# Optimization experiments

Measured on AMD Instinct MI355X. Metric: run time of the kernel, lower is better.

## Reference

```python
import jax, jax.numpy as jnp
import numpy as np

NUM_ROIS = 100
FLAT = NUM_ROIS * NUM_ROIS
B = 16
EPS_LN = 1e-5
NEG_SLOPE = 0.2
MASK_NEG = -1e9


def _normal(key, shape, scale):
    return (jax.random.normal(key, shape, dtype=jnp.float32) * scale)


def setup_inputs() -> dict:
    key = jax.random.key(0)
    ks = jax.random.split(key, 32)
    inp = {}
    inp["raw_fc_flat"] = jax.random.normal(ks[0], (B, FLAT), dtype=jnp.float32)
    # graph builder Linear(FLAT, FLAT)
    inp["gb_W"] = _normal(ks[1], (FLAT, FLAT), 1.0 / np.sqrt(FLAT))
    inp["gb_b"] = jnp.zeros((FLAT,), jnp.float32)
    # feature enhancer: Linear(2,8) -> GELU -> Linear(8,16) -> LayerNorm(16)
    inp["fe_W1"] = _normal(ks[2], (2, 8), 1.0 / np.sqrt(2))
    inp["fe_b1"] = jnp.zeros((8,), jnp.float32)
    inp["fe_W2"] = _normal(ks[3], (8, 16), 1.0 / np.sqrt(8))
    inp["fe_b2"] = jnp.zeros((16,), jnp.float32)
    inp["fe_g"] = jnp.ones((16,), jnp.float32)
    inp["fe_beta"] = jnp.zeros((16,), jnp.float32)
    # GATv2 layer 1: in=16, C=128, H=8, concat
    H1, C1 = 8, 128
    inp["Wl1"] = _normal(ks[4], (16, H1 * C1), 1.0 / np.sqrt(16))
    inp["bl1"] = jnp.zeros((H1 * C1,), jnp.float32)
    inp["Wr1"] = _normal(ks[5], (16, H1 * C1), 1.0 / np.sqrt(16))
    inp["br1"] = jnp.zeros((H1 * C1,), jnp.float32)
    inp["att1"] = _normal(ks[6], (H1, C1), 1.0 / np.sqrt(C1))
    inp["bias1"] = jnp.zeros((H1 * C1,), jnp.float32)
    # GATv2 layer 2: in=1024, C=256, H=4, concat
    H2, C2 = 4, 256
    inp["Wl2"] = _normal(ks[7], (1024, H2 * C2), 1.0 / np.sqrt(1024))
    inp["bl2"] = jnp.zeros((H2 * C2,), jnp.float32)
    inp["Wr2"] = _normal(ks[8], (1024, H2 * C2), 1.0 / np.sqrt(1024))
    inp["br2"] = jnp.zeros((H2 * C2,), jnp.float32)
    inp["att2"] = _normal(ks[9], (H2, C2), 1.0 / np.sqrt(C2))
    inp["bias2"] = jnp.zeros((H2 * C2,), jnp.float32)
    # GATv2 layer 3: in=1024, C=128, H=1, concat=False
    H3, C3 = 1, 128
    inp["Wl3"] = _normal(ks[10], (1024, H3 * C3), 1.0 / np.sqrt(1024))
    inp["bl3"] = jnp.zeros((H3 * C3,), jnp.float32)
    inp["Wr3"] = _normal(ks[11], (1024, H3 * C3), 1.0 / np.sqrt(1024))
    inp["br3"] = jnp.zeros((H3 * C3,), jnp.float32)
    inp["att3"] = _normal(ks[12], (H3, C3), 1.0 / np.sqrt(C3))
    inp["bias3"] = jnp.zeros((C3,), jnp.float32)
    return inp


def _gelu(x):
    return jax.nn.gelu(x, approximate=False)


def _gatv2(x, mask, Wl, bl, Wr, br, att, bias, concat):
    # x: [B,N,Fin], mask: [B,N,N] bool, mask[b,i,j] = edge j->i exists (i = target)
    b, n, _ = x.shape
    h, c = att.shape
    xl = (x @ Wl + bl).reshape(b, n, h, c)  # source / message features
    xr = (x @ Wr + br).reshape(b, n, h, c)  # target features
    # GATv2 score: e[b,h,i,j] = att_h . LeakyReLU(xl[b,j,h] + xr[b,i,h])
    g = jax.nn.leaky_relu(xl[:, None, :, :, :] + xr[:, :, None, :, :], NEG_SLOPE)  # [B,i,j,H,C]
    e = jnp.einsum('bijhc,hc->bhij', g, att)
    e = jnp.where(mask[:, None], e, MASK_NEG)
    alpha = jax.nn.softmax(e, axis=-1)
    alpha = jnp.where(mask[:, None], alpha, 0.0)  # zero rows with no neighbors
    out = jnp.einsum('bhij,bjhc->bihc', alpha, xl)  # [B,N,H,C]
    out = out.reshape(b, n, h * c) if concat else out.mean(axis=2)
    return out + bias


def reference(raw_fc_flat, gb_W, gb_b, fe_W1, fe_b1, fe_W2, fe_b2, fe_g, fe_beta,
              Wl1, bl1, Wr1, br1, att1, bias1,
              Wl2, bl2, Wr2, br2, att2, bias2,
              Wl3, bl3, Wr3, br3, att3, bias3):
    bs = raw_fc_flat.shape[0]
    n = NUM_ROIS
    # --- build_graph ---
    adj = jax.nn.sigmoid(raw_fc_flat @ gb_W + gb_b).reshape(bs, n, n)
    adj = (adj + jnp.swapaxes(adj, 1, 2)) * 0.5
    m = adj.mean(axis=2)                 # per-row mean   [B,N]
    s = adj.std(axis=2, ddof=1)          # unbiased std   [B,N]
    b_ft = jnp.stack([m, s + 1e-6], axis=-1)  # [B,N,2]
    hft = _gelu(b_ft @ fe_W1 + fe_b1) @ fe_W2 + fe_b2  # [B,N,16]
    mu = hft.mean(axis=-1, keepdims=True)
    var = hft.var(axis=-1, keepdims=True)
    x = (hft - mu) / jnp.sqrt(var + EPS_LN) * fe_g + fe_beta  # node features [B,N,16]
    thr = jnp.quantile(adj.reshape(bs, -1), 0.75, axis=1)      # per-sample threshold [B]
    mask = adj > thr[:, None, None]  # symmetric edge mask [B,N,N]
    eye = jnp.eye(n, dtype=bool)[None]
    mask_sl = mask | eye  # layers 2,3 add self loops
    # --- GAT stack (eval mode: dropout = identity) ---
    x = _gelu(_gatv2(x, mask, Wl1, bl1, Wr1, br1, att1, bias1, concat=True))
    x = _gelu(_gatv2(x, mask_sl, Wl2, bl2, Wr2, br2, att2, bias2, concat=True))
    x = _gelu(_gatv2(x, mask_sl, Wl3, bl3, Wr3, br3, att3, bias3, concat=False))
    # global mean pool over nodes of each graph
    return x.mean(axis=1)  # [B, gnn_output_dim]
```

## Files before the change

### kernel.cpp

```cpp
#include <hip/hip_runtime.h>
#include <cmath>

#define BATCH 16
#define NROI 100
#define FLATD 10000
#define NTILE 10

typedef __attribute__((ext_vector_type(8))) short s16x8;
typedef __attribute__((ext_vector_type(4))) short s16x4;
typedef __attribute__((ext_vector_type(4))) float f32x4;

__device__ __forceinline__ float sigmoidf(float x) { return 1.0f / (1.0f + expf(-x)); }
__device__ __forceinline__ float geluf(float x) { return 0.5f * x * (1.0f + erff(x * 0.70710678118654752f)); }
__device__ __forceinline__ short f2bf(float x) {
    union { float f; unsigned u; } v; v.f = x;
    unsigned r = v.u + 0x7FFF + ((v.u >> 16) & 1);
    return (short)(r >> 16);
}

__global__ __launch_bounds__(256) void prep_misc(const float* __restrict__ A, float* __restrict__ At,
                                                 const float* __restrict__ Wl2, const float* __restrict__ Wr2,
                                                 const float* __restrict__ Wl3, const float* __restrict__ Wr3,
                                                 short* __restrict__ Wt2l, short* __restrict__ Wt2r,
                                                 short* __restrict__ Wt3l, short* __restrict__ Wt3r) {
    __shared__ float t[32][33];
    int bid = blockIdx.x;
    int tid = threadIdx.x;
    if (bid < 625) {
        int e = bid * 256 + tid;
        At[e] = A[(size_t)(e & 15) * FLATD + (e >> 4)];
        return;
    }
    int r = bid - 625;
    const float* in; short* out; int N, xb, yb;
    if (r < 1024)      { in = Wl2; out = Wt2l; N = 1024; xb = r & 31; yb = r >> 5; }
    else if (r < 2048) { r -= 1024; in = Wr2; out = Wt2r; N = 1024; xb = r & 31; yb = r >> 5; }
    else if (r < 2176) { r -= 2048; in = Wl3; out = Wt3l; N = 128;  xb = r & 3;  yb = r >> 2; }
    else               { r -= 2176; in = Wr3; out = Wt3r; N = 128;  xb = r & 3;  yb = r >> 2; }
    int n0 = xb * 32, k0 = yb * 32;
    int tx = tid & 31, ty = tid >> 5;
#pragma unroll
    for (int i = 0; i < 32; i += 8)
        t[ty + i][tx] = in[(size_t)(k0 + ty + i) * N + n0 + tx];
    __syncthreads();
#pragma unroll
    for (int i = 0; i < 32; i += 8)
        out[(size_t)(n0 + ty + i) * 1024 + k0 + tx] = f2bf(t[tx][ty + i]);
}

__global__ __launch_bounds__(256) void gemm1_part(const float* __restrict__ At, const float* __restrict__ W,
                                                  float* __restrict__ part) {
    int col = blockIdx.x * 512 + threadIdx.x * 2;
    if (col >= FLATD) return;
    int ky = blockIdx.y;
    int k0 = ky * 400, k1 = k0 + 400;
    float acc0[16], acc1[16];
#pragma unroll
    for (int m = 0; m < 16; ++m) { acc0[m] = 0.f; acc1[m] = 0.f; }
#pragma unroll 4
    for (int k = k0; k < k1; ++k) {
        float2 w = *reinterpret_cast<const float2*>(W + (size_t)k * FLATD + col);
        const float* a = At + k * 16;
#pragma unroll
        for (int m = 0; m < 16; ++m) { acc0[m] += a[m] * w.x; acc1[m] += a[m] * w.y; }
    }
    float* dst = part + (size_t)ky * 160000;
#pragma unroll
    for (int m = 0; m < 16; ++m) {
        float2 o; o.x = acc0[m]; o.y = acc1[m];
        *reinterpret_cast<float2*>(dst + (size_t)m * FLATD + col) = o;
    }
}

__global__ __launch_bounds__(256) void sym_stats(const float* __restrict__ part, const float* __restrict__ gbb,
                                                 float* __restrict__ adjsym, float* __restrict__ bft) {
    __shared__ float s_adj[50][NROI + 1];
    int b = blockIdx.x;
    int i0 = blockIdx.y * 50;
    for (int idx = threadIdx.x; idx < 50 * NROI; idx += 256) {
        int ii = idx / NROI, j = idx % NROI;
        int i = i0 + ii;
        size_t e1 = (size_t)b * FLATD + i * NROI + j;
        size_t e2 = (size_t)b * FLATD + j * NROI + i;
        float s1 = 0.f, s2 = 0.f;
#pragma unroll
        for (int p = 0; p < 25; ++p) {
            s1 += part[(size_t)p * 160000 + e1];
            s2 += part[(size_t)p * 160000 + e2];
        }
        float v = 0.5f * (sigmoidf(s1 + gbb[i * NROI + j]) + sigmoidf(s2 + gbb[j * NROI + i]));
        s_adj[ii][j] = v;
        adjsym[e1] = v;
    }
    __syncthreads();
    if (threadIdx.x < 50) {
        int i = threadIdx.x;
        float sum = 0.f, sumsq = 0.f;
        for (int j = 0; j < NROI; ++j) { float v = s_adj[i][j]; sum += v; sumsq += v * v; }
        float mean = sum * 0.01f;
        float var = (sumsq - sum * sum * 0.01f) * (1.0f / 99.0f);
        var = fmaxf(var, 0.f);
        bft[(b * NROI + i0 + i) * 2 + 0] = mean;
        bft[(b * NROI + i0 + i) * 2 + 1] = sqrtf(var) + 1e-6f;
    }
}

__global__ __launch_bounds__(512) void quant_enh(const float* __restrict__ adjsym, float* __restrict__ thr,
                                                 const float* __restrict__ bft,
                                                 const float* __restrict__ W1, const float* __restrict__ b1,
                                                 const float* __restrict__ W2, const float* __restrict__ b2,
                                                 const float* __restrict__ g, const float* __restrict__ beta,
                                                 float* __restrict__ x0) {
    if (blockIdx.x >= 16) {
        int idx = (blockIdx.x - 16) * 512 + threadIdx.x;
        if (idx >= BATCH * NROI) return;
        float f0 = bft[idx * 2 + 0], f1 = bft[idx * 2 + 1];
        float h8[8];
#pragma unroll
        for (int u = 0; u < 8; ++u) h8[u] = geluf(W1[u] * f0 + W1[8 + u] * f1 + b1[u]);
        float o[16];
        float mu = 0.f;
#pragma unroll
        for (int v = 0; v < 16; ++v) {
            float t = b2[v];
#pragma unroll
            for (int u = 0; u < 8; ++u) t += h8[u] * W2[u * 16 + v];
            o[v] = t; mu += t;
        }
        mu *= (1.0f / 16.0f);
        float var = 0.f;
#pragma unroll
        for (int v = 0; v < 16; ++v) { float d = o[v] - mu; var += d * d; }
        var *= (1.0f / 16.0f);
        float inv = rsqrtf(var + 1e-5f);
#pragma unroll
        for (int v = 0; v < 16; ++v) x0[idx * 16 + v] = (o[v] - mu) * inv * g[v] + beta[v];
        return;
    }
    __shared__ int red[8];
    __shared__ float redf[8];
    int b = blockIdx.x;
    int tid = threadIdx.x;
    unsigned v[20];
    const unsigned* src = (const unsigned*)(adjsym + (size_t)b * FLATD);
#pragma unroll
    for (int s = 0; s < 20; ++s) {
        int idx = s * 512 + tid;
        v[s] = (idx < FLATD) ? src[idx] : 0x7F800000u;
    }
    int rem = 7499;
    unsigned prefix = 0;
    for (int bit = 30; bit >= 0; --bit) {
        unsigned pshift = prefix >> (bit + 1);
        int c = 0;
#pragma unroll
        for (int s = 0; s < 20; ++s) {
            unsigned x = v[s];
            c += (((x >> (bit + 1)) == pshift) && (((x >> bit) & 1u) == 0u)) ? 1 : 0;
        }
#pragma unroll
        for (int o = 32; o > 0; o >>= 1) c += __shfl_down(c, o, 64);
        if ((tid & 63) == 0) red[tid >> 6] = c;
        __syncthreads();
        int total = red[0] + red[1] + red[2] + red[3] + red[4] + red[5] + red[6] + red[7];
        __syncthreads();
        if (rem >= total) { rem -= total; prefix |= 1u << bit; }
    }
    union { unsigned u; float f; } cv; cv.u = prefix;
    float v0 = cv.f;
    int cle = 0;
    float mg = 3.4e38f;
#pragma unroll
    for (int s = 0; s < 20; ++s) {
        union { unsigned u; float f; } w; w.u = v[s];
        float f = w.f;
        cle += (f <= v0) ? 1 : 0;
        if (f > v0) mg = fminf(mg, f);
    }
#pragma unroll
    for (int o = 32; o > 0; o >>= 1) {
        cle += __shfl_down(cle, o, 64);
        mg = fminf(mg, __shfl_down(mg, o, 64));
    }
    if ((tid & 63) == 0) { red[tid >> 6] = cle; redf[tid >> 6] = mg; }
    __syncthreads();
    if (tid == 0) {
        int tc = 0; float tm = 3.4e38f;
#pragma unroll
        for (int w = 0; w < 8; ++w) { tc += red[w]; tm = fminf(tm, redf[w]); }
        float v1 = (tc >= 7501) ? v0 : tm;
        thr[b] = v0 + 0.25f * (v1 - v0);
    }
}

__global__ __launch_bounds__(256) void proj_gemm(const float* __restrict__ X,
                                                 const float* __restrict__ WL, const float* __restrict__ WR,
                                                 const float* __restrict__ biasL, const float* __restrict__ biasR,
                                                 float* __restrict__ outL, float* __restrict__ outR,
                                                 int K, int Nout) {
    __shared__ float As[16][65];
    __shared__ float Bs[16][128];
    const float* W = blockIdx.z ? WR : WL;
    const float* bias = blockIdx.z ? biasR : biasL;
    float* out = blockIdx.z ? outR : outL;
    int tid = threadIdx.x;
    int tm = tid & 15, tn = tid >> 4;
    int m0 = blockIdx.x * 64, n0 = blockIdx.y * 128;
    float acc[4][8];
#pragma unroll
    for (int r = 0; r < 4; ++r)
#pragma unroll
        for (int c = 0; c < 8; ++c) acc[r][c] = 0.f;
    for (int k0 = 0; k0 < K; k0 += 16) {
        for (int e = tid; e < 64 * 16; e += 256) {
            int kk = e & 15, mm = e >> 4;
            As[kk][mm] = X[(size_t)(m0 + mm) * K + k0 + kk];
        }
        for (int e = tid; e < 16 * 128; e += 256) {
            int nn = e & 127, kk = e >> 7;
            Bs[kk][nn] = W[(size_t)(k0 + kk) * Nout + n0 + nn];
        }
        __syncthreads();
#pragma unroll
        for (int kk = 0; kk < 16; ++kk) {
            float a[4], bb[8];
#pragma unroll
            for (int r = 0; r < 4; ++r) a[r] = As[kk][tm * 4 + r];
#pragma unroll
            for (int c = 0; c < 8; ++c) bb[c] = Bs[kk][tn * 8 + c];
#pragma unroll
            for (int r = 0; r < 4; ++r)
#pragma unroll
                for (int c = 0; c < 8; ++c) acc[r][c] += a[r] * bb[c];
        }
        __syncthreads();
    }
#pragma unroll
    for (int r = 0; r < 4; ++r)
#pragma unroll
        for (int c = 0; c < 8; ++c)
            out[(size_t)(m0 + tm * 4 + r) * Nout + n0 + tn * 8 + c] = acc[r][c] + bias[n0 + tn * 8 + c];
}

__global__ __launch_bounds__(256) void mfma_proj(const short* __restrict__ Xb,
                                                 const short* __restrict__ WtL, const short* __restrict__ WtR,
                                                 const float* __restrict__ biasL, const float* __restrict__ biasR,
                                                 float* __restrict__ outL, float* __restrict__ outR,
                                                 int K, int N) {
    __shared__ short As[64 * 72];
    __shared__ short Bs[64 * 72];
    const short* Wt  = blockIdx.z ? WtR : WtL;
    const float* bias = blockIdx.z ? biasR : biasL;
    float* out = blockIdx.z ? outR : outL;
    int m0 = blockIdx.x * 64, n0 = blockIdx.y * 64;
    int tid = threadIdx.x;
    int row = tid >> 2, part = tid & 3;
    int lane = tid & 63, wave = tid >> 6;
    int wm = wave & 1, wn = wave >> 1;
    int quad = lane >> 4, l16 = lane & 15;
    f32x4 acc00 = {}, acc01 = {}, acc10 = {}, acc11 = {};
    const short* gA = Xb + (size_t)(m0 + row) * K + part * 16;
    const short* gB = Wt + (size_t)(n0 + row) * K + part * 16;
    short* sA = As + row * 72 + part * 16;
    short* sB = Bs + row * 72 + part * 16;
    const short* fA = As + (wm * 32 + l16) * 72 + quad * 8;
    const short* fB = Bs + (wn * 32 + l16) * 72 + quad * 8;
    for (int k0 = 0; k0 < K; k0 += 64) {
        *reinterpret_cast<s16x8*>(sA)     = *reinterpret_cast<const s16x8*>(gA + k0);
        *reinterpret_cast<s16x8*>(sA + 8) = *reinterpret_cast<const s16x8*>(gA + k0 + 8);
        *reinterpret_cast<s16x8*>(sB)     = *reinterpret_cast<const s16x8*>(gB + k0);
        *reinterpret_cast<s16x8*>(sB + 8) = *reinterpret_cast<const s16x8*>(gB + k0 + 8);
        __syncthreads();
#pragma unroll
        for (int ks = 0; ks < 2; ++ks) {
            s16x8 a0 = *reinterpret_cast<const s16x8*>(fA + ks * 32);
            s16x8 a1 = *reinterpret_cast<const s16x8*>(fA + ks * 32 + 16 * 72);
            s16x8 b0 = *reinterpret_cast<const s16x8*>(fB + ks * 32);
            s16x8 b1 = *reinterpret_cast<const s16x8*>(fB + ks * 32 + 16 * 72);
            acc00 = __builtin_amdgcn_mfma_f32_16x16x32_bf16(a0, b0, acc00, 0, 0, 0);
            acc01 = __builtin_amdgcn_mfma_f32_16x16x32_bf16(a0, b1, acc01, 0, 0, 0);
            acc10 = __builtin_amdgcn_mfma_f32_16x16x32_bf16(a1, b0, acc10, 0, 0, 0);
            acc11 = __builtin_amdgcn_mfma_f32_16x16x32_bf16(a1, b1, acc11, 0, 0, 0);
        }
        __syncthreads();
    }
#pragma unroll
    for (int tm = 0; tm < 2; ++tm)
#pragma unroll
        for (int tn = 0; tn < 2; ++tn) {
            const f32x4& a = tm == 0 ? (tn == 0 ? acc00 : acc01) : (tn == 0 ? acc10 : acc11);
            int mbase = m0 + wm * 32 + tm * 16 + quad * 4;
            int n = n0 + wn * 32 + tn * 16 + l16;
            float bv = bias[n];
#pragma unroll
            for (int r = 0; r < 4; ++r)
                out[(size_t)(mbase + r) * N + n] = a[r] + bv;
        }
}

__global__ __launch_bounds__(128) void score_softmax(const float* __restrict__ xl, const float* __restrict__ xr,
                                                     const float* __restrict__ att, const float* __restrict__ adjsym,
                                                     const float* __restrict__ thr, float* __restrict__ alpha,
                                                     int H, int C, int self_loop) {
    __shared__ float s_abs[NTILE][105];
    __shared__ float dl_lds[104];
    int bh = blockIdx.x;
    int b = bh / H, h = bh % H;
    int i0 = blockIdx.y * NTILE;
    int j = threadIdx.x;
    const float* xlrow = xl + ((size_t)(b * NROI + (j < NROI ? j : 0)) * H + h) * C;
    const float* xrbase = xr + ((size_t)(b * NROI + i0) * H + h) * C;
    const float* atth = att + h * C;
    float acc[NTILE];
    float dl = 0.f;
#pragma unroll
    for (int i = 0; i < NTILE; ++i) acc[i] = 0.f;
    for (int cc = 0; cc < C; cc += 32) {
        float xlr[32];
#pragma unroll
        for (int t = 0; t < 32; ++t) xlr[t] = xlrow[cc + t];
        const float* attp = atth + cc;
#pragma unroll
        for (int t = 0; t < 32; ++t) dl += attp[t] * xlr[t];
#pragma unroll
        for (int i = 0; i < NTILE; ++i) {
            const float* xrrow = xrbase + (size_t)i * H * C + cc;
            float s = 0.f;
#pragma unroll
            for (int t = 0; t < 32; ++t) s += attp[t] * fabsf(xlr[t] + xrrow[t]);
            acc[i] += s;
        }
    }
    if (j < NROI) {
        dl_lds[j] = dl;
#pragma unroll
        for (int i = 0; i < NTILE; ++i) s_abs[i][j] = acc[i];
    }
    __syncthreads();
    int t = threadIdx.x;
    int i = t >> 2, q = t & 3;
    if (i < NTILE) {
        int gi = i0 + i;
        int c4 = C >> 2;
        const float* xrrow = xr + ((size_t)(b * NROI + gi) * H + h) * C + q * c4;
        const float* attq = atth + q * c4;
        float dr = 0.f;
        for (int c = 0; c < c4; ++c) dr += attq[c] * xrrow[c];
        dr += __shfl_xor(dr, 1, 64);
        dr += __shfl_xor(dr, 2, 64);
        float tb = thr[b];
        const float* arow = adjsym + (size_t)b * FLATD + gi * NROI + q * 25;
        float em[25];
        float mx = -3.0e38f;
#pragma unroll
        for (int k = 0; k < 25; ++k) {
            int jj = q * 25 + k;
            float e = 0.6f * (dl_lds[jj] + dr) + 0.4f * s_abs[i][jj];
            bool edge = (arow[k] > tb) || (self_loop && (jj == gi));
            float v = edge ? e : -1.0e9f;
            em[k] = v;
            mx = fmaxf(mx, v);
        }
        mx = fmaxf(mx, __shfl_xor(mx, 1, 64));
        mx = fmaxf(mx, __shfl_xor(mx, 2, 64));
        float sum = 0.f;
#pragma unroll
        for (int k = 0; k < 25; ++k) {
            em[k] = (em[k] > -0.5e9f) ? expf(em[k] - mx) : 0.f;
            sum += em[k];
        }
        sum += __shfl_xor(sum, 1, 64);
        sum += __shfl_xor(sum, 2, 64);
        float inv = (sum > 0.f) ? 1.0f / sum : 0.f;
        float* ab = alpha + (size_t)(b * H + h) * FLATD + gi;
#pragma unroll
        for (int k = 0; k < 25; ++k) ab[(q * 25 + k) * NROI] = em[k] * inv;
    }
}

__global__ __launch_bounds__(128) void agg_kernel(const float* __restrict__ xl, const float* __restrict__ alpha,
                                                  const float* __restrict__ bias, short* __restrict__ yout,
                                                  float* __restrict__ pool_out, int H, int C, int pool) {
    __shared__ float s_xl[NROI * 128];
    int bh = blockIdx.x;
    int b = bh / H, h = bh % H;
    int ch = blockIdx.y;
    int i0 = blockIdx.z * 25;
    int tid = threadIdx.x;
    for (int e = tid; e < NROI * 128; e += 128) {
        int jj = e >> 7, t = e & 127;
        s_xl[e] = xl[((size_t)(b * NROI + jj) * H + h) * C + ch * 128 + t];
    }
    __syncthreads();
    int cglob = ch * 128 + tid;
    float bval = bias[h * C + cglob];
    const float* ap = alpha + (size_t)(b * H + h) * FLATD;
    float pacc = 0.f;
    for (int ib = 0; ib < 25; ib += 8) {
        int nb = (25 - ib) >= 8 ? 8 : (25 - ib);
        float acc[8] = {0.f, 0.f, 0.f, 0.f, 0.f, 0.f, 0.f, 0.f};
        if (nb == 8) {
            for (int jj = 0; jj < NROI; ++jj) {
                float xlv = s_xl[jj * 128 + tid];
                const float* ar = ap + jj * NROI + i0 + ib;
#pragma unroll
                for (int t = 0; t < 8; ++t) acc[t] += ar[t] * xlv;
            }
        } else {
            for (int jj = 0; jj < NROI; ++jj)
                acc[0] += ap[jj * NROI + i0 + ib] * s_xl[jj * 128 + tid];
        }
        for (int t = 0; t < nb; ++t) {
            int gi = i0 + ib + t;
            float v = geluf(acc[t] + bval);
            if (pool) pacc += 0.01f * v;
            else yout[((size_t)(b * NROI + gi) * H + h) * C + cglob] = f2bf(v);
        }
    }
    if (pool) atomicAdd(pool_out + b * 128 + cglob, pacc);
}

extern "C" void kernel_launch(void* const* d_in, const int* in_sizes, int n_in,
                              void* d_out, int out_size, void* d_ws, size_t ws_size,
                              hipStream_t stream) {
    const float* A    = (const float*)d_in[0];
    const float* gbW  = (const float*)d_in[1];
    const float* gbb  = (const float*)d_in[2];
    const float* feW1 = (const float*)d_in[3];
    const float* feb1 = (const float*)d_in[4];
    const float* feW2 = (const float*)d_in[5];
    const float* feb2 = (const float*)d_in[6];
    const float* feg  = (const float*)d_in[7];
    const float* febt = (const float*)d_in[8];
    const float* Wl1  = (const float*)d_in[9];
    const float* bl1  = (const float*)d_in[10];
    const float* Wr1  = (const float*)d_in[11];
    const float* br1  = (const float*)d_in[12];
    const float* att1 = (const float*)d_in[13];
    const float* bias1= (const float*)d_in[14];
    const float* Wl2  = (const float*)d_in[15];
    const float* bl2  = (const float*)d_in[16];
    const float* Wr2  = (const float*)d_in[17];
    const float* br2  = (const float*)d_in[18];
    const float* att2 = (const float*)d_in[19];
    const float* bias2= (const float*)d_in[20];
    const float* Wl3  = (const float*)d_in[21];
    const float* bl3  = (const float*)d_in[22];
    const float* Wr3  = (const float*)d_in[23];
    const float* br3  = (const float*)d_in[24];
    const float* att3 = (const float*)d_in[25];
    const float* bias3= (const float*)d_in[26];

    float* ws = (float*)d_ws;
    float* At    = ws + 0;
    float* adj   = ws + 160000;
    float* thr   = ws + 320000;
    float* bft   = ws + 320016;
    float* x0    = ws + 323216;
    float* xlbuf = ws + 348816;
    float* xrbuf = ws + 1987216;
    float* alpha = ws + 3625616;
    short* Xb    = (short*)(ws + 4905616);
    short* Wt2l  = (short*)(ws + 5724816);
    short* Wt2r  = (short*)(ws + 6249104);
    short* Wt3l  = (short*)(ws + 6773392);
    short* Wt3r  = (short*)(ws + 6838928);
    float* prep  = ws + 6904464;

    hipMemsetAsync(d_out, 0, (size_t)out_size * sizeof(float), stream);

    prep_misc<<<2929, 256, 0, stream>>>(A, At, Wl2, Wr2, Wl3, Wr3, Wt2l, Wt2r, Wt3l, Wt3r);
    gemm1_part<<<dim3(20, 25), 256, 0, stream>>>(At, gbW, prep);
    sym_stats<<<dim3(BATCH, 2), 256, 0, stream>>>(prep, gbb, adj, bft);
    quant_enh<<<20, 512, 0, stream>>>(adj, thr, bft, feW1, feb1, feW2, feb2, feg, febt, x0);

    proj_gemm<<<dim3(25, 8, 2), 256, 0, stream>>>(x0, Wl1, Wr1, bl1, br1, xlbuf, xrbuf, 16, 1024);
    score_softmax<<<dim3(128, 10), 128, 0, stream>>>(xlbuf, xrbuf, att1, adj, thr, alpha, 8, 128, 0);
    agg_kernel<<<dim3(128, 1, 4), 128, 0, stream>>>(xlbuf, alpha, bias1, Xb, nullptr, 8, 128, 0);

    mfma_proj<<<dim3(25, 16, 2), 256, 0, stream>>>(Xb, Wt2l, Wt2r, bl2, br2, xlbuf, xrbuf, 1024, 1024);
    score_softmax<<<dim3(64, 10), 128, 0, stream>>>(xlbuf, xrbuf, att2, adj, thr, alpha, 4, 256, 1);
    agg_kernel<<<dim3(64, 2, 4), 128, 0, stream>>>(xlbuf, alpha, bias2, Xb, nullptr, 4, 256, 0);

    mfma_proj<<<dim3(25, 2, 2), 256, 0, stream>>>(Xb, Wt3l, Wt3r, bl3, br3, xlbuf, xrbuf, 1024, 128);
    score_softmax<<<dim3(16, 10), 128, 0, stream>>>(xlbuf, xrbuf, att3, adj, thr, alpha, 1, 128, 1);
    agg_kernel<<<dim3(16, 1, 4), 128, 0, stream>>>(xlbuf, alpha, bias3, nullptr, (float*)d_out, 1, 128, 1);
}
```

Measured before the change: 997.4 us.

## Fuse GAT score/softmax with aggregation and stage A transpose in shared memory

New measurement: 940.0 us. 1.06x faster.

```diff
diff --git a/kernel.cpp b/kernel.cpp
--- a/kernel.cpp
+++ b/kernel.cpp
@@ -18,20 +18,13 @@
     return (short)(r >> 16);
 }
 
-__global__ __launch_bounds__(256) void prep_misc(const float* __restrict__ A, float* __restrict__ At,
-                                                 const float* __restrict__ Wl2, const float* __restrict__ Wr2,
-                                                 const float* __restrict__ Wl3, const float* __restrict__ Wr3,
-                                                 short* __restrict__ Wt2l, short* __restrict__ Wt2r,
-                                                 short* __restrict__ Wt3l, short* __restrict__ Wt3r) {
+__global__ __launch_bounds__(256) void prep_w(const float* __restrict__ Wl2, const float* __restrict__ Wr2,
+                                              const float* __restrict__ Wl3, const float* __restrict__ Wr3,
+                                              short* __restrict__ Wt2l, short* __restrict__ Wt2r,
+                                              short* __restrict__ Wt3l, short* __restrict__ Wt3r) {
     __shared__ float t[32][33];
-    int bid = blockIdx.x;
-    int tid = threadIdx.x;
-    if (bid < 625) {
-        int e = bid * 256 + tid;
-        At[e] = A[(size_t)(e & 15) * FLATD + (e >> 4)];
-        return;
-    }
-    int r = bid - 625;
+    int r = blockIdx.x;
+    int tid = threadIdx.x;
     const float* in; short* out; int N, xb, yb;
     if (r < 1024)      { in = Wl2; out = Wt2l; N = 1024; xb = r & 31; yb = r >> 5; }
     else if (r < 2048) { r -= 1024; in = Wr2; out = Wt2r; N = 1024; xb = r & 31; yb = r >> 5; }
@@ -48,19 +41,26 @@
         out[(size_t)(n0 + ty + i) * 1024 + k0 + tx] = f2bf(t[tx][ty + i]);
 }
 
-__global__ __launch_bounds__(256) void gemm1_part(const float* __restrict__ At, const float* __restrict__ W,
+__global__ __launch_bounds__(256) void gemm1_part(const float* __restrict__ A, const float* __restrict__ W,
                                                   float* __restrict__ part) {
-    int col = blockIdx.x * 512 + threadIdx.x * 2;
+    __shared__ float sA[400][16];
+    int ky = blockIdx.y;
+    int k0 = ky * 400;
+    int tid = threadIdx.x;
+    for (int e = tid; e < 16 * 400; e += 256) {
+        int m = e / 400, kk = e - m * 400;
+        sA[kk][m] = A[(size_t)m * FLATD + k0 + kk];
+    }
+    __syncthreads();
+    int col = blockIdx.x * 512 + tid * 2;
     if (col >= FLATD) return;
-    int ky = blockIdx.y;
-    int k0 = ky * 400, k1 = k0 + 400;
     float acc0[16], acc1[16];
 #pragma unroll
     for (int m = 0; m < 16; ++m) { acc0[m] = 0.f; acc1[m] = 0.f; }
 #pragma unroll 4
-    for (int k = k0; k < k1; ++k) {
-        float2 w = *reinterpret_cast<const float2*>(W + (size_t)k * FLATD + col);
-        const float* a = At + k * 16;
+    for (int kk = 0; kk < 400; ++kk) {
+        float2 w = *reinterpret_cast<const float2*>(W + (size_t)(k0 + kk) * FLATD + col);
+        const float* a = sA[kk];
 #pragma unroll
         for (int m = 0; m < 16; ++m) { acc0[m] += a[m] * w.x; acc1[m] += a[m] * w.y; }
     }
@@ -298,48 +298,73 @@
         }
 }
 
-__global__ __launch_bounds__(128) void score_softmax(const float* __restrict__ xl, const float* __restrict__ xr,
-                                                     const float* __restrict__ att, const float* __restrict__ adjsym,
-                                                     const float* __restrict__ thr, float* __restrict__ alpha,
-                                                     int H, int C, int self_loop) {
-    __shared__ float s_abs[NTILE][105];
-    __shared__ float dl_lds[104];
+__global__ __launch_bounds__(256) void gat_fused(const float* __restrict__ xl, const float* __restrict__ xr,
+                                                 const float* __restrict__ att, const float* __restrict__ adjsym,
+                                                 const float* __restrict__ thr, const float* __restrict__ bias,
+                                                 short* __restrict__ yout, float* __restrict__ pool_out,
+                                                 int H, int C, int self_loop, int pool) {
+    __shared__ float s_abs2[2][NTILE][104];
+    __shared__ float dl2[2][104];
+    __shared__ float p_lds[NTILE][104];
+    __shared__ float s_xr[NTILE][256];
     int bh = blockIdx.x;
     int b = bh / H, h = bh % H;
     int i0 = blockIdx.y * NTILE;
-    int j = threadIdx.x;
-    const float* xlrow = xl + ((size_t)(b * NROI + (j < NROI ? j : 0)) * H + h) * C;
-    const float* xrbase = xr + ((size_t)(b * NROI + i0) * H + h) * C;
+    int tid = threadIdx.x;
     const float* atth = att + h * C;
-    float acc[NTILE];
-    float dl = 0.f;
-#pragma unroll
-    for (int i = 0; i < NTILE; ++i) acc[i] = 0.f;
-    for (int cc = 0; cc < C; cc += 32) {
-        float xlr[32];
-#pragma unroll
-        for (int t = 0; t < 32; ++t) xlr[t] = xlrow[cc + t];
-        const float* attp = atth + cc;
-#pragma unroll
-        for (int t = 0; t < 32; ++t) dl += attp[t] * xlr[t];
-#pragma unroll
-        for (int i = 0; i < NTILE; ++i) {
-            const float* xrrow = xrbase + (size_t)i * H * C + cc;
-            float s = 0.f;
-#pragma unroll
-            for (int t = 0; t < 32; ++t) s += attp[t] * fabsf(xlr[t] + xrrow[t]);
-            acc[i] += s;
-        }
-    }
-    if (j < NROI) {
-        dl_lds[j] = dl;
-#pragma unroll
-        for (int i = 0; i < NTILE; ++i) s_abs[i][j] = acc[i];
-    }
-    __syncthreads();
-    int t = threadIdx.x;
-    int i = t >> 2, q = t & 3;
-    if (i < NTILE) {
+
+    for (int e = tid; e < NTILE * C; e += 256) {
+        int i = e / C, c = e - i * C;
+        s_xr[i][c] = xr[((size_t)(b * NROI + i0 + i) * H + h) * C + c];
+    }
+    __syncthreads();
+
+    {
+        int j = tid & 127;
+        int cg = tid >> 7;
+        int Ch = C >> 1;
+        int cbase = cg * Ch;
+        const float* xlrow = xl + ((size_t)(b * NROI + (j < NROI ? j : 0)) * H + h) * C + cbase;
+        const float* attp0 = atth + cbase;
+        float acc[NTILE];
+        float dl = 0.f;
+#pragma unroll
+        for (int i = 0; i < NTILE; ++i) acc[i] = 0.f;
+        for (int cc = 0; cc < Ch; cc += 32) {
+            float xlr[32];
+#pragma unroll
+            for (int t = 0; t < 32; t += 4) {
+                float4 v = *reinterpret_cast<const float4*>(xlrow + cc + t);
+                xlr[t] = v.x; xlr[t + 1] = v.y; xlr[t + 2] = v.z; xlr[t + 3] = v.w;
+            }
+            const float* attp = attp0 + cc;
+#pragma unroll
+            for (int t = 0; t < 32; ++t) dl += attp[t] * xlr[t];
+#pragma unroll
+            for (int i = 0; i < NTILE; ++i) {
+                const float* xrp = &s_xr[i][cbase + cc];
+                float s = 0.f;
+#pragma unroll
+                for (int t = 0; t < 32; t += 4) {
+                    float4 xv = *reinterpret_cast<const float4*>(xrp + t);
+                    s += attp[t + 0] * fabsf(xlr[t + 0] + xv.x);
+                    s += attp[t + 1] * fabsf(xlr[t + 1] + xv.y);
+                    s += attp[t + 2] * fabsf(xlr[t + 2] + xv.z);
+                    s += attp[t + 3] * fabsf(xlr[t + 3] + xv.w);
+                }
+                acc[i] += s;
+            }
+        }
+        if (j < NROI) {
+            dl2[cg][j] = dl;
+#pragma unroll
+            for (int i = 0; i < NTILE; ++i) s_abs2[cg][i][j] = acc[i];
+        }
+    }
+    __syncthreads();
+
+    if (tid < NTILE * 4) {
+        int i = tid >> 2, q = tid & 3;
         int gi = i0 + i;
         int c4 = C >> 2;
         const float* xrrow = xr + ((size_t)(b * NROI + gi) * H + h) * C + q * c4;
@@ -355,7 +380,8 @@
 #pragma unroll
         for (int k = 0; k < 25; ++k) {
             int jj = q * 25 + k;
-            float e = 0.6f * (dl_lds[jj] + dr) + 0.4f * s_abs[i][jj];
+            float e = 0.6f * (dl2[0][jj] + dl2[1][jj] + dr)
+                    + 0.4f * (s_abs2[0][i][jj] + s_abs2[1][i][jj]);
             bool edge = (arow[k] > tb) || (self_loop && (jj == gi));
             float v = edge ? e : -1.0e9f;
             em[k] = v;
@@ -372,52 +398,42 @@
         sum += __shfl_xor(sum, 1, 64);
         sum += __shfl_xor(sum, 2, 64);
         float inv = (sum > 0.f) ? 1.0f / sum : 0.f;
-        float* ab = alpha + (size_t)(b * H + h) * FLATD + gi;
-#pragma unroll
-        for (int k = 0; k < 25; ++k) ab[(q * 25 + k) * NROI] = em[k] * inv;
-    }
-}
-
-__global__ __launch_bounds__(128) void agg_kernel(const float* __restrict__ xl, const float* __restrict__ alpha,
-                                                  const float* __restrict__ bias, short* __restrict__ yout,
-                                                  float* __restrict__ pool_out, int H, int C, int pool) {
-    __shared__ float s_xl[NROI * 128];
-    int bh = blockIdx.x;
-    int b = bh / H, h = bh % H;
-    int ch = blockIdx.y;
-    int i0 = blockIdx.z * 25;
-    int tid = threadIdx.x;
-    for (int e = tid; e < NROI * 128; e += 128) {
-        int jj = e >> 7, t = e & 127;
-        s_xl[e] = xl[((size_t)(b * NROI + jj) * H + h) * C + ch * 128 + t];
-    }
-    __syncthreads();
-    int cglob = ch * 128 + tid;
-    float bval = bias[h * C + cglob];
-    const float* ap = alpha + (size_t)(b * H + h) * FLATD;
-    float pacc = 0.f;
-    for (int ib = 0; ib < 25; ib += 8) {
-        int nb = (25 - ib) >= 8 ? 8 : (25 - ib);
-        float acc[8] = {0.f, 0.f, 0.f, 0.f, 0.f, 0.f, 0.f, 0.f};
-        if (nb == 8) {
-            for (int jj = 0; jj < NROI; ++jj) {
-                float xlv = s_xl[jj * 128 + tid];
-                const float* ar = ap + jj * NROI + i0 + ib;
-#pragma unroll
-                for (int t = 0; t < 8; ++t) acc[t] += ar[t] * xlv;
+#pragma unroll
+        for (int k = 0; k < 25; ++k) p_lds[i][q * 25 + k] = em[k] * inv;
+    }
+    __syncthreads();
+
+    for (int c = tid; c < C; c += 256) {
+        float acc[NTILE];
+#pragma unroll
+        for (int i = 0; i < NTILE; ++i) acc[i] = 0.f;
+        const float* xbase = xl + ((size_t)(b * NROI) * H + h) * C + c;
+        size_t jstride = (size_t)H * C;
+        for (int j0 = 0; j0 < NROI; j0 += 4) {
+            float x0v = xbase[(j0 + 0) * jstride];
+            float x1v = xbase[(j0 + 1) * jstride];
+            float x2v = xbase[(j0 + 2) * jstride];
+            float x3v = xbase[(j0 + 3) * jstride];
+#pragma unroll
+            for (int i = 0; i < NTILE; ++i) {
+                float4 p = *reinterpret_cast<const float4*>(&p_lds[i][j0]);
+                acc[i] += p.x * x0v + p.y * x1v + p.z * x2v + p.w * x3v;
             }
+        }
+        float bval = bias[h * C + c];
+        if (pool) {
+            float pacc = 0.f;
+#pragma unroll
+            for (int i = 0; i < NTILE; ++i) pacc += 0.01f * geluf(acc[i] + bval);
+            atomicAdd(pool_out + b * 128 + c, pacc);
         } else {
-            for (int jj = 0; jj < NROI; ++jj)
-                acc[0] += ap[jj * NROI + i0 + ib] * s_xl[jj * 128 + tid];
-        }
-        for (int t = 0; t < nb; ++t) {
-            int gi = i0 + ib + t;
-            float v = geluf(acc[t] + bval);
-            if (pool) pacc += 0.01f * v;
-            else yout[((size_t)(b * NROI + gi) * H + h) * C + cglob] = f2bf(v);
-        }
-    }
-    if (pool) atomicAdd(pool_out + b * 128 + cglob, pacc);
+#pragma unroll
+            for (int i = 0; i < NTILE; ++i) {
+                int gi = i0 + i;
+                yout[((size_t)(b * NROI + gi) * H + h) * C + c] = f2bf(geluf(acc[i] + bval));
+            }
+        }
+    }
 }
 
 extern "C" void kernel_launch(void* const* d_in, const int* in_sizes, int n_in,
@@ -452,37 +468,32 @@
     const float* bias3= (const float*)d_in[26];
 
     float* ws = (float*)d_ws;
-    float* At    = ws + 0;
-    float* adj   = ws + 160000;
-    float* thr   = ws + 320000;
-    float* bft   = ws + 320016;
-    float* x0    = ws + 323216;
-    float* xlbuf = ws + 348816;
-    float* xrbuf = ws + 1987216;
-    float* alpha = ws + 3625616;
-    short* Xb    = (short*)(ws + 4905616);
-    short* Wt2l  = (short*)(ws + 5724816);
-    short* Wt2r  = (short*)(ws + 6249104);
-    short* Wt3l  = (short*)(ws + 6773392);
-    short* Wt3r  = (short*)(ws + 6838928);
-    float* prep  = ws + 6904464;
+    float* adj   = ws + 0;
+    float* thr   = ws + 160000;
+    float* bft   = ws + 160016;
+    float* x0    = ws + 163216;
+    float* xlbuf = ws + 188816;
+    float* xrbuf = ws + 1827216;
+    short* Xb    = (short*)(ws + 3465616);
+    short* Wt2l  = (short*)(ws + 4284816);
+    short* Wt2r  = (short*)(ws + 4809104);
+    short* Wt3l  = (short*)(ws + 5333392);
+    short* Wt3r  = (short*)(ws + 5398928);
+    float* prep  = ws + 5464464;
 
     hipMemsetAsync(d_out, 0, (size_t)out_size * sizeof(float), stream);
 
-    prep_misc<<<2929, 256, 0, stream>>>(A, At, Wl2, Wr2, Wl3, Wr3, Wt2l, Wt2r, Wt3l, Wt3r);
-    gemm1_part<<<dim3(20, 25), 256, 0, stream>>>(At, gbW, prep);
+    gemm1_part<<<dim3(20, 25), 256, 0, stream>>>(A, gbW, prep);
+    prep_w<<<2304, 256, 0, stream>>>(Wl2, Wr2, Wl3, Wr3, Wt2l, Wt2r, Wt3l, Wt3r);
     sym_stats<<<dim3(BATCH, 2), 256, 0, stream>>>(prep, gbb, adj, bft);
     quant_enh<<<20, 512, 0, stream>>>(adj, thr, bft, feW1, feb1, feW2, feb2, feg, febt, x0);
 
     proj_gemm<<<dim3(25, 8, 2), 256, 0, stream>>>(x0, Wl1, Wr1, bl1, br1, xlbuf, xrbuf, 16, 1024);
-    score_softmax<<<dim3(128, 10), 128, 0, stream>>>(xlbuf, xrbuf, att1, adj, thr, alpha, 8, 128, 0);
-    agg_kernel<<<dim3(128, 1, 4), 128, 0, stream>>>(xlbuf, alpha, bias1, Xb, nullptr, 8, 128, 0);
+    gat_fused<<<dim3(128, 10), 256, 0, stream>>>(xlbuf, xrbuf, att1, adj, thr, bias1, Xb, nullptr, 8, 128, 0, 0);
 
     mfma_proj<<<dim3(25, 16, 2), 256, 0, stream>>>(Xb, Wt2l, Wt2r, bl2, br2, xlbuf, xrbuf, 1024, 1024);
-    score_softmax<<<dim3(64, 10), 128, 0, stream>>>(xlbuf, xrbuf, att2, adj, thr, alpha, 4, 256, 1);
-    agg_kernel<<<dim3(64, 2, 4), 128, 0, stream>>>(xlbuf, alpha, bias2, Xb, nullptr, 4, 256, 0);
+    gat_fused<<<dim3(64, 10), 256, 0, stream>>>(xlbuf, xrbuf, att2, adj, thr, bias2, Xb, nullptr, 4, 256, 1, 0);
 
     mfma_proj<<<dim3(25, 2, 2), 256, 0, stream>>>(Xb, Wt3l, Wt3r, bl3, br3, xlbuf, xrbuf, 1024, 128);
-    score_softmax<<<dim3(16, 10), 128, 0, stream>>>(xlbuf, xrbuf, att3, adj, thr, alpha, 1, 128, 1);
-    agg_kernel<<<dim3(16, 1, 4), 128, 0, stream>>>(xlbuf, alpha, bias3, nullptr, (float*)d_out, 1, 128, 1);
-}
+    gat_fused<<<dim3(16, 10), 256, 0, stream>>>(xlbuf, xrbuf, att3, adj, thr, bias3, nullptr, (float*)d_out, 1, 128, 1, 1);
+}
```
